# Kernel optimization log

Measured on AMD Instinct MI355X. Metric: run time of the kernel, lower is better.

## Reference

```python
import jax, jax.numpy as jnp
import numpy as np

EMB = 128
N_LIG = 32768
N_REC = 262144
NUM_GRAPHS = 1024
E_LIG = 327680
E_REC = 2097152
LIG_DIMS = [119, 9, 11, 12, 9, 5, 8, 2, 2]
NUM_LAYERS = 3
BN_EPS = 1e-5


def setup_inputs() -> dict:
    key = jax.random.key(0)
    ks = iter(jax.random.split(key, 64))

    lig_x = jnp.stack(
        [jax.random.randint(next(ks), (N_LIG,), 0, d) for d in LIG_DIMS], axis=1
    )  # [N_lig, 9] categorical atom features
    atom_offsets = jnp.asarray(np.cumsum([0] + LIG_DIMS[:-1]), dtype=jnp.int32)
    atom_emb = jax.random.normal(next(ks), (sum(LIG_DIMS), EMB), jnp.float32) * 0.1

    rec_x_int = jax.random.randint(next(ks), (N_REC,), 0, 20)
    rec_x_float = jax.random.normal(next(ks), (N_REC, 199), jnp.float32)
    rec_emb1 = jax.random.normal(next(ks), (20, EMB), jnp.float32) * 0.1
    rec_w = jax.random.normal(next(ks), (199, EMB), jnp.float32) * 0.05
    rec_b = jnp.zeros((EMB,), jnp.float32)

    lig_edge_index = jax.random.randint(next(ks), (2, E_LIG), 0, N_LIG)
    rec_edge_index = jax.random.randint(next(ks), (2, E_REC), 0, N_REC)
    lig_batch = jnp.repeat(jnp.arange(NUM_GRAPHS), N_LIG // NUM_GRAPHS)
    rec_batch = jnp.repeat(jnp.arange(NUM_GRAPHS), N_REC // NUM_GRAPHS)

    def layer_params():
        W = jax.random.normal(next(ks), (NUM_LAYERS, EMB, EMB), jnp.float32) * (1.0 / np.sqrt(EMB))
        b = jnp.zeros((NUM_LAYERS, EMB), jnp.float32)
        gamma = jnp.ones((NUM_LAYERS, EMB), jnp.float32)
        beta = jnp.zeros((NUM_LAYERS, EMB), jnp.float32)
        return W, b, gamma, beta

    lig_W, lig_b, lig_gamma, lig_beta = layer_params()
    rec_W, rec_bc, rec_gamma, rec_beta = layer_params()

    out_w1 = jax.random.normal(next(ks), (2 * EMB, EMB), jnp.float32) * (1.0 / np.sqrt(2 * EMB))
    out_b1 = jnp.zeros((EMB,), jnp.float32)
    out_w2 = jax.random.normal(next(ks), (EMB, 1), jnp.float32) * (1.0 / np.sqrt(EMB))
    out_b2 = jnp.zeros((1,), jnp.float32)

    return dict(
        lig_x=lig_x, rec_x_int=rec_x_int, rec_x_float=rec_x_float,
        lig_edge_index=lig_edge_index, rec_edge_index=rec_edge_index,
        lig_batch=lig_batch, rec_batch=rec_batch, atom_offsets=atom_offsets,
        atom_emb=atom_emb, rec_emb1=rec_emb1, rec_w=rec_w, rec_b=rec_b,
        lig_W=lig_W, lig_b=lig_b, lig_gamma=lig_gamma, lig_beta=lig_beta,
        rec_W=rec_W, rec_bc=rec_bc, rec_gamma=rec_gamma, rec_beta=rec_beta,
        out_w1=out_w1, out_b1=out_b1, out_w2=out_w2, out_b2=out_b2,
    )


def gcn_layer(x, edge_index, W, b, gamma, beta):
    """GCNConv (sym-norm, self loops) -> BatchNorm (batch stats) -> ReLU."""
    n = x.shape[0]
    h = x @ W  # [N, EMB]
    loops = jnp.arange(n)
    src = jnp.concatenate([edge_index[0], loops])
    dst = jnp.concatenate([edge_index[1], loops])
    deg = jax.ops.segment_sum(jnp.ones_like(dst, dtype=h.dtype), dst, num_segments=n)
    dinv = jax.lax.rsqrt(jnp.maximum(deg, 1.0))  # deg >= 1 with self loops
    msg = h[src] * (dinv[src] * dinv[dst])[:, None]  # gather + normalize
    out = jax.ops.segment_sum(msg, dst, num_segments=n) + b
    mu = out.mean(axis=0)
    var = out.var(axis=0)
    out = (out - mu) * jax.lax.rsqrt(var + BN_EPS) * gamma + beta
    return jax.nn.relu(out)


def scatter_mean(x, seg, num_segments):
    s = jax.ops.segment_sum(x, seg, num_segments=num_segments)
    cnt = jax.ops.segment_sum(jnp.ones((x.shape[0],), x.dtype), seg, num_segments=num_segments)
    return s / jnp.maximum(cnt, 1.0)[:, None]


def reference(lig_x, rec_x_int, rec_x_float, lig_edge_index, rec_edge_index,
              lig_batch, rec_batch, atom_offsets, atom_emb, rec_emb1, rec_w, rec_b,
              lig_W, lig_b, lig_gamma, lig_beta, rec_W, rec_bc, rec_gamma, rec_beta,
              out_w1, out_b1, out_w2, out_b2):
    # Node encoders
    lig_h = atom_emb[lig_x + atom_offsets[None, :]].sum(axis=1)        # [N_lig, EMB]
    rec_h = rec_emb1[rec_x_int] + rec_x_float @ rec_w + rec_b          # [N_rec, EMB]

    for l in range(NUM_LAYERS):
        lig_h = gcn_layer(lig_h, lig_edge_index, lig_W[l], lig_b[l], lig_gamma[l], lig_beta[l])
        rec_h = gcn_layer(rec_h, rec_edge_index, rec_W[l], rec_bc[l], rec_gamma[l], rec_beta[l])

    lig_feat = scatter_mean(lig_h, lig_batch, NUM_GRAPHS)
    rec_feat = scatter_mean(rec_h, rec_batch, NUM_GRAPHS)
    z = jnp.concatenate([lig_feat, rec_feat], axis=1)                  # [B, 2*EMB]
    z = jax.nn.relu(z @ out_w1 + out_b1)
    return (z @ out_w2 + out_b2).squeeze(-1)                            # [B]
```

## Files before the change

kernel.cpp:

```cpp
#include <hip/hip_runtime.h>
#include <hip/hip_bf16.h>
#include <cstdint>
#include <cstddef>

#define EMB 128
#define NLIG 32768
#define NREC 262144
#define NGRAPH 1024
#define ELIG 327680
#define EREC 2097152
#define BN_EPS 1e-5f

typedef unsigned short ushort_t;
typedef short bf16x8 __attribute__((ext_vector_type(8)));
typedef float f32x4 __attribute__((ext_vector_type(4)));

__device__ __forceinline__ float bf2f(ushort_t u) {
  union { unsigned int i; float f; } v;
  v.i = ((unsigned int)u) << 16;
  return v.f;
}
__device__ __forceinline__ ushort_t f2bf(float f) {
  __hip_bfloat16 h = __float2bfloat16(f);
  union { __hip_bfloat16 h; ushort_t u; } v;
  v.h = h;
  return v.u;
}


__global__ __launch_bounds__(256)
void gk_count(const int* __restrict__ dst, int* __restrict__ cnt, int E) {
  int e = blockIdx.x * 256 + threadIdx.x;
  if (e < E) atomicAdd(&cnt[dst[e]], 1);
}

__global__ __launch_bounds__(256)
void gk_scan1(const int* __restrict__ cnt, int* __restrict__ off,
              int* __restrict__ bsum, int n) {
  __shared__ int sm[256];
  int t = threadIdx.x;
  int base = blockIdx.x * 1024 + t * 4;
  int v0 = (base + 0 < n) ? cnt[base + 0] : 0;
  int v1 = (base + 1 < n) ? cnt[base + 1] : 0;
  int v2 = (base + 2 < n) ? cnt[base + 2] : 0;
  int v3 = (base + 3 < n) ? cnt[base + 3] : 0;
  int loc = v0 + v1 + v2 + v3;
  sm[t] = loc;
  __syncthreads();
  for (int o = 1; o < 256; o <<= 1) {
    int x = (t >= o) ? sm[t - o] : 0;
    __syncthreads();
    sm[t] += x;
    __syncthreads();
  }
  int run = sm[t] - loc;
  if (base + 0 < n) off[base + 0] = run;
  run += v0;
  if (base + 1 < n) off[base + 1] = run;
  run += v1;
  if (base + 2 < n) off[base + 2] = run;
  run += v2;
  if (base + 3 < n) off[base + 3] = run;
  if (t == 255) bsum[blockIdx.x] = sm[255];
}

__global__ __launch_bounds__(256)
void gk_scan2(int* __restrict__ bsum, int nb) {
  __shared__ int sm[256];
  int t = threadIdx.x;
  int v = (t < nb) ? bsum[t] : 0;
  sm[t] = v;
  __syncthreads();
  for (int o = 1; o < 256; o <<= 1) {
    int x = (t >= o) ? sm[t - o] : 0;
    __syncthreads();
    sm[t] += x;
    __syncthreads();
  }
  if (t < nb) bsum[t] = sm[t] - v;
}

__global__ __launch_bounds__(256)
void gk_scan3(int* __restrict__ off, const int* __restrict__ bsum, int n, int E) {
  int i = blockIdx.x * 256 + threadIdx.x;
  if (i < n) off[i] += bsum[i >> 10];
  if (i == 0) off[n] = E;
}

__global__ __launch_bounds__(256)
void gk_copy(int* __restrict__ d, const int* __restrict__ s, int n) {
  int i = blockIdx.x * 256 + threadIdx.x;
  if (i < n) d[i] = s[i];
}

__global__ __launch_bounds__(256)
void gk_fill(const int* __restrict__ src, const int* __restrict__ dst,
             int* __restrict__ cur, int* __restrict__ csr, int E) {
  int e = blockIdx.x * 256 + threadIdx.x;
  if (e < E) {
    int d = dst[e];
    int pos = atomicAdd(&cur[d], 1);
    csr[pos] = src[e];
  }
}

__global__ __launch_bounds__(256)
void gk_dinv(const int* __restrict__ off, float* __restrict__ dinv, int n) {
  int i = blockIdx.x * 256 + threadIdx.x;
  if (i < n) dinv[i] = rsqrtf((float)(off[i + 1] - off[i] + 1));
}


__global__ __launch_bounds__(128)
void gk_ligenc(const int* __restrict__ lig_x, const int* __restrict__ offs,
               const float* __restrict__ emb, ushort_t* __restrict__ A) {
  __shared__ int idx[9];
  int i = blockIdx.x;
  int c = threadIdx.x;
  if (c < 9) idx[c] = lig_x[i * 9 + c] + offs[c];
  __syncthreads();
  float acc = 0.f;
#pragma unroll
  for (int f = 0; f < 9; ++f) acc += emb[(size_t)idx[f] * EMB + c];
  A[(size_t)i * EMB + c] = f2bf(acc);
}

__global__ __launch_bounds__(256)
void gk_recw2(const float* __restrict__ W, ushort_t* __restrict__ Wt) {
  int idx = blockIdx.x * 256 + threadIdx.x;
  if (idx < 128 * 224) {
    int c = idx / 224, k = idx - c * 224;
    Wt[idx] = (k < 199) ? f2bf(W[(size_t)k * 128 + c]) : (ushort_t)0;
  }
}

__global__ __launch_bounds__(256)
void gk_xcast(const float* __restrict__ X, ushort_t* __restrict__ Xb) {
  const int ITEMS = NREC * 25;
  int stride = gridDim.x * 256;
  for (int v = blockIdx.x * 256 + threadIdx.x; v < ITEMS; v += stride) {
    int row = v / 25, sub = v - row * 25;
    int k0 = sub * 8;
    const float* xr = X + (size_t)row * 199 + k0;
    ushort_t tmp[8];
#pragma unroll
    for (int j = 0; j < 8; ++j) {
      float f = (k0 + j < 199) ? xr[j] : 0.f;
      tmp[j] = f2bf(f);
    }
    *(uint4*)(Xb + (size_t)row * 200 + k0) = *(uint4*)tmp;
  }
}

__global__ __launch_bounds__(256)
void gk_recenc2(const ushort_t* __restrict__ Xb, const int* __restrict__ xi,
                const float* __restrict__ emb1, const ushort_t* __restrict__ Wt,
                const float* __restrict__ b, ushort_t* __restrict__ A) {
  int t = threadIdx.x;
  int row0 = blockIdx.x * 128;
  int w = t >> 6, lane = t & 63;
  int m = lane & 15, quad = lane >> 4;
  int rbase = w * 32;
  int rA = row0 + rbase + m;
  int rB = rA + 16;

  f32x4 acc[2][8];
#pragma unroll
  for (int rt = 0; rt < 2; ++rt)
#pragma unroll
    for (int ct = 0; ct < 8; ++ct) acc[rt][ct] = (f32x4){0.f, 0.f, 0.f, 0.f};

  const ushort_t* xpA = Xb + (size_t)rA * 200 + quad * 8;
  const ushort_t* xpB = Xb + (size_t)rB * 200 + quad * 8;
  const ushort_t* wp = Wt + (size_t)m * 224 + quad * 8;

  for (int ch = 0; ch < 7; ++ch) {
    bf16x8 a0 = *(const bf16x8*)(xpA + ch * 32);
    bf16x8 a1 = *(const bf16x8*)(xpB + ch * 32);
#pragma unroll
    for (int ct = 0; ct < 8; ++ct) {
      bf16x8 bb = *(const bf16x8*)(wp + (size_t)ct * 16 * 224 + ch * 32);
      acc[0][ct] = __builtin_amdgcn_mfma_f32_16x16x32_bf16(a0, bb, acc[0][ct], 0, 0, 0);
      acc[1][ct] = __builtin_amdgcn_mfma_f32_16x16x32_bf16(a1, bb, acc[1][ct], 0, 0, 0);
    }
  }

  float bcol[8];
#pragma unroll
  for (int ct = 0; ct < 8; ++ct) bcol[ct] = b[ct * 16 + m];
#pragma unroll
  for (int rt = 0; rt < 2; ++rt) {
    int rb = row0 + rbase + rt * 16 + quad * 4;
#pragma unroll
    for (int rr = 0; rr < 4; ++rr) {
      int row = rb + rr;
      const float* e = emb1 + (size_t)xi[row] * 128;
#pragma unroll
      for (int ct = 0; ct < 8; ++ct) {
        int c = ct * 16 + m;
        float v = acc[rt][ct][rr] + bcol[ct] + e[c];
        A[(size_t)row * 128 + c] = f2bf(v);
      }
    }
  }
}

__global__ __launch_bounds__(256)
void gk_prep(const float* __restrict__ W, const float* __restrict__ stats,
             const float* __restrict__ gamma, const float* __restrict__ beta,
             float inv_n, int donorm, ushort_t* __restrict__ Wt,
             float* __restrict__ bnscl, float* __restrict__ bnsh) {
  int idx = blockIdx.x * 256 + threadIdx.x;
  if (idx < 128) {
    if (donorm) {
      float mu = stats[idx] * inv_n;
      float var = stats[128 + idx] * inv_n - mu * mu;
      float s = gamma[idx] * rsqrtf(var + BN_EPS);
      bnscl[idx] = s;
      bnsh[idx] = beta[idx] - mu * s;
    } else {
      bnscl[idx] = 1.f;
      bnsh[idx] = 0.f;
    }
  }
  int c = idx >> 7, k = idx & 127;
  Wt[(size_t)c * 128 + k] = f2bf(W[(size_t)k * 128 + c]);
}

__global__ __launch_bounds__(256)
void gk_mm(const ushort_t* __restrict__ Xb, const ushort_t* __restrict__ Wt,
           const float* __restrict__ bnscl, const float* __restrict__ bnsh,
           int donorm, const float* __restrict__ dinv,
           ushort_t* __restrict__ gb) {
  __shared__ ushort_t Xs[128 * 128];
  __shared__ ushort_t Ws[128 * 128];
  int t = threadIdx.x;
  int row0 = blockIdx.x * 128;

  for (int i = t; i < 2048; i += 256) {
    int r = i >> 4, cc = i & 15;
    union { uint4 v; ushort_t s[8]; } u;
    u.v = *(const uint4*)(Xb + (size_t)(row0 + r) * 128 + cc * 8);
    if (donorm) {
#pragma unroll
      for (int j = 0; j < 8; ++j) {
        int k = cc * 8 + j;
        float f = fmaf(bf2f(u.s[j]), bnscl[k], bnsh[k]);
        f = f > 0.f ? f : 0.f;
        u.s[j] = f2bf(f);
      }
    }
    *(uint4*)&Xs[r * 128 + ((cc ^ (r & 15)) * 8)] = u.v;
  }
  for (int i = t; i < 2048; i += 256) {
    int c = i >> 4, cc = i & 15;
    uint4 u = *(const uint4*)(Wt + (size_t)c * 128 + cc * 8);
    *(uint4*)&Ws[c * 128 + ((cc ^ (c & 15)) * 8)] = u;
  }
  __syncthreads();

  int w = t >> 6, lane = t & 63;
  int m = lane & 15, quad = lane >> 4;
  int rbase = w * 32;

  f32x4 acc[2][8];
#pragma unroll
  for (int rt = 0; rt < 2; ++rt)
#pragma unroll
    for (int ct = 0; ct < 8; ++ct) acc[rt][ct] = (f32x4){0.f, 0.f, 0.f, 0.f};

#pragma unroll
  for (int kc8 = 0; kc8 < 16; kc8 += 4) {
    int ck = (kc8 + quad) ^ m;
    bf16x8 a0 = *(const bf16x8*)&Xs[(rbase + m) * 128 + ck * 8];
    bf16x8 a1 = *(const bf16x8*)&Xs[(rbase + 16 + m) * 128 + ck * 8];
#pragma unroll
    for (int ct = 0; ct < 8; ++ct) {
      bf16x8 b = *(const bf16x8*)&Ws[(ct * 16 + m) * 128 + ck * 8];
      acc[0][ct] = __builtin_amdgcn_mfma_f32_16x16x32_bf16(a0, b, acc[0][ct], 0, 0, 0);
      acc[1][ct] = __builtin_amdgcn_mfma_f32_16x16x32_bf16(a1, b, acc[1][ct], 0, 0, 0);
    }
  }

#pragma unroll
  for (int rt = 0; rt < 2; ++rt) {
    int rb = row0 + rbase + rt * 16 + quad * 4;
    float d0 = dinv[rb + 0], d1 = dinv[rb + 1];
    float d2 = dinv[rb + 2], d3 = dinv[rb + 3];
#pragma unroll
    for (int ct = 0; ct < 8; ++ct) {
      int c = ct * 16 + m;
      gb[(size_t)(rb + 0) * 128 + c] = f2bf(acc[rt][ct][0] * d0);
      gb[(size_t)(rb + 1) * 128 + c] = f2bf(acc[rt][ct][1] * d1);
      gb[(size_t)(rb + 2) * 128 + c] = f2bf(acc[rt][ct][2] * d2);
      gb[(size_t)(rb + 3) * 128 + c] = f2bf(acc[rt][ct][3] * d3);
    }
  }
}


struct Quad {
  int i0, i1, i2, i3;
  float m0, m1, m2, m3;
};

__device__ __forceinline__ Quad load_quad(const int* __restrict__ csr,
                                          int e, int e1, int safe) {
  Quad q;
  int c0 = (e + 0 < e1) ? e + 0 : safe;
  int c1 = (e + 1 < e1) ? e + 1 : safe;
  int c2 = (e + 2 < e1) ? e + 2 : safe;
  int c3 = (e + 3 < e1) ? e + 3 : safe;
  q.i0 = csr[c0];
  q.i1 = csr[c1];
  q.i2 = csr[c2];
  q.i3 = csr[c3];
  q.m0 = (e + 0 < e1) ? 1.f : 0.f;
  q.m1 = (e + 1 < e1) ? 1.f : 0.f;
  q.m2 = (e + 2 < e1) ? 1.f : 0.f;
  q.m3 = (e + 3 < e1) ? 1.f : 0.f;
  return q;
}

__device__ __forceinline__ void gather4(const ushort_t* __restrict__ g, int c0,
                                        const Quad& q, unsigned int* v) {
  v[0] = *(const unsigned int*)(g + (size_t)q.i0 * 128 + c0);
  v[1] = *(const unsigned int*)(g + (size_t)q.i1 * 128 + c0);
  v[2] = *(const unsigned int*)(g + (size_t)q.i2 * 128 + c0);
  v[3] = *(const unsigned int*)(g + (size_t)q.i3 * 128 + c0);
}

__device__ __forceinline__ void consume4(float2& acc, const Quad& q,
                                         const unsigned int* v) {
  float lo0 = bf2f((ushort_t)(v[0] & 0xffffu)), hi0 = bf2f((ushort_t)(v[0] >> 16));
  float lo1 = bf2f((ushort_t)(v[1] & 0xffffu)), hi1 = bf2f((ushort_t)(v[1] >> 16));
  float lo2 = bf2f((ushort_t)(v[2] & 0xffffu)), hi2 = bf2f((ushort_t)(v[2] >> 16));
  float lo3 = bf2f((ushort_t)(v[3] & 0xffffu)), hi3 = bf2f((ushort_t)(v[3] >> 16));
  acc.x = fmaf(lo0, q.m0, acc.x); acc.y = fmaf(hi0, q.m0, acc.y);
  acc.x = fmaf(lo1, q.m1, acc.x); acc.y = fmaf(hi1, q.m1, acc.y);
  acc.x = fmaf(lo2, q.m2, acc.x); acc.y = fmaf(hi2, q.m2, acc.y);
  acc.x = fmaf(lo3, q.m3, acc.x); acc.y = fmaf(hi3, q.m3, acc.y);
}

__global__ __launch_bounds__(256)
void gk_agg(const ushort_t* __restrict__ g, const int* __restrict__ off,
            const int* __restrict__ csr, const float* __restrict__ dinv,
            ushort_t* __restrict__ outb, float* __restrict__ stats) {
  __shared__ float ls[128];
  __shared__ float lss[128];
  int t = threadIdx.x;
  int slot = t >> 6;
  int lane = t & 63;
  int c0 = lane * 2;
  int i0 = blockIdx.x * 32;

  if (t < 128) { ls[t] = 0.f; lss[t] = 0.f; }
  __syncthreads();

  float sx = 0.f, sy = 0.f, ssx = 0.f, ssy = 0.f;

  for (int p = 0; p < 4; ++p) {
    int rA = i0 + slot * 2 + p * 8;
    int rB = rA + 1;
    int eA = off[rA], eA1 = off[rA + 1];
    int eB1 = off[rB + 1];
    int eB = eA1;
    float dA = dinv[rA], dB = dinv[rB];
    unsigned int uA = *(const unsigned int*)(g + (size_t)rA * 128 + c0);
    unsigned int uB = *(const unsigned int*)(g + (size_t)rB * 128 + c0);
    float2 accA = make_float2(bf2f((ushort_t)(uA & 0xffffu)),
                              bf2f((ushort_t)(uA >> 16)));
    float2 accB = make_float2(bf2f((ushort_t)(uB & 0xffffu)),
                              bf2f((ushort_t)(uB >> 16)));
    int safeA = (eA1 > eA) ? eA1 - 1 : 0;
    int safeB = (eB1 > eB) ? eB1 - 1 : 0;

    Quad qA = load_quad(csr, eA, eA1, safeA);
    Quad qB = load_quad(csr, eB, eB1, safeB);
    unsigned int vA[4], vB[4];
    gather4(g, c0, qA, vA);
    gather4(g, c0, qB, vB);
    int e_A = eA + 4, e_B = eB + 4;

    while (e_A < eA1 || e_B < eB1) {
      bool an = e_A < eA1;
      bool bn = e_B < eB1;
      Quad qA2, qB2;
      unsigned int wA[4], wB[4];
      if (an) {
        qA2 = load_quad(csr, e_A, eA1, safeA);
        gather4(g, c0, qA2, wA);
      }
      if (bn) {
        qB2 = load_quad(csr, e_B, eB1, safeB);
        gather4(g, c0, qB2, wB);
      }
      consume4(accA, qA, vA);
      consume4(accB, qB, vB);
      if (an) {
        qA = qA2; vA[0] = wA[0]; vA[1] = wA[1]; vA[2] = wA[2]; vA[3] = wA[3];
        e_A += 4;
      } else {
        qA.m0 = qA.m1 = qA.m2 = qA.m3 = 0.f;
      }
      if (bn) {
        qB = qB2; vB[0] = wB[0]; vB[1] = wB[1]; vB[2] = wB[2]; vB[3] = wB[3];
        e_B += 4;
      } else {
        qB.m0 = qB.m1 = qB.m2 = qB.m3 = 0.f;
      }
    }
    consume4(accA, qA, vA);
    consume4(accB, qB, vB);

    accA.x *= dA; accA.y *= dA;
    accB.x *= dB; accB.y *= dB;
    unsigned int oA = (unsigned int)f2bf(accA.x) | ((unsigned int)f2bf(accA.y) << 16);
    unsigned int oB = (unsigned int)f2bf(accB.x) | ((unsigned int)f2bf(accB.y) << 16);
    *(unsigned int*)(outb + (size_t)rA * 128 + c0) = oA;
    *(unsigned int*)(outb + (size_t)rB * 128 + c0) = oB;
    sx += accA.x + accB.x;
    sy += accA.y + accB.y;
    ssx = fmaf(accA.x, accA.x, ssx); ssx = fmaf(accB.x, accB.x, ssx);
    ssy = fmaf(accA.y, accA.y, ssy); ssy = fmaf(accB.y, accB.y, ssy);
  }

  atomicAdd(&ls[c0 + 0], sx);
  atomicAdd(&ls[c0 + 1], sy);
  atomicAdd(&lss[c0 + 0], ssx);
  atomicAdd(&lss[c0 + 1], ssy);
  __syncthreads();
  if (t < 128) {
    atomicAdd(&stats[t], ls[t]);
    atomicAdd(&stats[t + 128], lss[t]);
  }
}

__global__ __launch_bounds__(128)
void gk_pool(const ushort_t* __restrict__ A, const float* __restrict__ stats,
             const float* __restrict__ gamma, const float* __restrict__ beta,
             float inv_n, float* __restrict__ z, int npg, int zoff) {
  int gidx = blockIdx.x;
  int c = threadIdx.x;
  float mu = stats[c] * inv_n;
  float var = stats[128 + c] * inv_n - mu * mu;
  float scl = gamma[c] * rsqrtf(var + BN_EPS);
  float be = beta[c];
  float sum = 0.f;
  int r0 = gidx * npg;
  for (int r = 0; r < npg; ++r) {
    float v = (bf2f(A[(size_t)(r0 + r) * 128 + c]) - mu) * scl + be;
    sum += v > 0.f ? v : 0.f;
  }
  z[(size_t)gidx * 256 + zoff + c] = sum * (1.0f / (float)npg);
}

__global__ __launch_bounds__(128)
void gk_mlp(const float* __restrict__ z, const float* __restrict__ w1,
            const float* __restrict__ b1, const float* __restrict__ w2,
            const float* __restrict__ b2, float* __restrict__ out) {
  __shared__ float zs[256];
  __shared__ float red[128];
  int gidx = blockIdx.x, t = threadIdx.x;
  zs[t] = z[(size_t)gidx * 256 + t];
  zs[t + 128] = z[(size_t)gidx * 256 + 128 + t];
  __syncthreads();
  float acc = b1[t];
  for (int k = 0; k < 256; ++k) acc += zs[k] * w1[(size_t)k * 128 + t];
  acc = (acc > 0.f ? acc : 0.f) * w2[t];
  red[t] = acc;
  __syncthreads();
  for (int o = 64; o > 0; o >>= 1) {
    if (t < o) red[t] += red[t + o];
    __syncthreads();
  }
  if (t == 0) out[gidx] = red[0] + b2[0];
}


extern "C" void kernel_launch(void* const* d_in, const int* in_sizes, int n_in,
                              void* d_out, int out_size, void* d_ws, size_t ws_size,
                              hipStream_t stream) {
  (void)in_sizes; (void)n_in; (void)out_size; (void)ws_size;
  const int*   lig_x       = (const int*)  d_in[0];
  const int*   rec_x_int   = (const int*)  d_in[1];
  const float* rec_x_float = (const float*)d_in[2];
  const int*   lig_ei      = (const int*)  d_in[3];
  const int*   rec_ei      = (const int*)  d_in[4];
  const int*   atom_off    = (const int*)  d_in[7];
  const float* atom_emb    = (const float*)d_in[8];
  const float* rec_emb1    = (const float*)d_in[9];
  const float* rec_w       = (const float*)d_in[10];
  const float* rec_b       = (const float*)d_in[11];
  const float* lig_W       = (const float*)d_in[12];
  const float* lig_gamma   = (const float*)d_in[14];
  const float* lig_beta    = (const float*)d_in[15];
  const float* rec_W       = (const float*)d_in[16];
  const float* rec_gamma   = (const float*)d_in[18];
  const float* rec_beta    = (const float*)d_in[19];
  const float* out_w1      = (const float*)d_in[20];
  const float* out_b1      = (const float*)d_in[21];
  const float* out_w2      = (const float*)d_in[22];
  const float* out_b2      = (const float*)d_in[23];
  float* out = (float*)d_out;

  char* p = (char*)d_ws;
  auto alloc = [&](size_t bytes) -> void* {
    void* r = p;
    p += (bytes + 255) & ~(size_t)255;
    return r;
  };
  ushort_t* Ab     = (ushort_t*)alloc((size_t)NREC * EMB * 2);
  ushort_t* Gb     = (ushort_t*)alloc((size_t)NREC * EMB * 2);
  ushort_t* Wtb    = (ushort_t*)alloc((size_t)EMB * EMB * 2);
  ushort_t* WtK    = (ushort_t*)alloc((size_t)EMB * 224 * 2);
  ushort_t* Xb2    = (ushort_t*)alloc(((size_t)NREC * 200 + 64) * 2);
  float* bnscl     = (float*)alloc(128 * 4);
  float* bnsh      = (float*)alloc(128 * 4);
  float* dinv_lig  = (float*)alloc((size_t)NLIG * 4);
  float* dinv_rec  = (float*)alloc((size_t)NREC * 4);
  int*   cnt_lig   = (int*)  alloc((size_t)NLIG * 4);
  int*   cnt_rec   = (int*)  alloc((size_t)NREC * 4);
  int*   off_lig   = (int*)  alloc((size_t)(NLIG + 1) * 4);
  int*   off_rec   = (int*)  alloc((size_t)(NREC + 1) * 4);
  int*   csr_lig   = (int*)  alloc((size_t)ELIG * 4);
  int*   csr_rec   = (int*)  alloc((size_t)EREC * 4);
  int*   bsum_lig  = (int*)  alloc(256 * 4);
  int*   bsum_rec  = (int*)  alloc(256 * 4);
  float* stats     = (float*)alloc(256 * 4);
  float* z         = (float*)alloc((size_t)NGRAPH * 256 * 4);

  hipMemsetAsync(cnt_lig, 0, (size_t)NLIG * 4, stream);
  hipMemsetAsync(cnt_rec, 0, (size_t)NREC * 4, stream);
  gk_count<<<ELIG / 256, 256, 0, stream>>>(lig_ei + ELIG, cnt_lig, ELIG);
  gk_count<<<EREC / 256, 256, 0, stream>>>(rec_ei + EREC, cnt_rec, EREC);
  gk_scan1<<<NLIG / 1024, 256, 0, stream>>>(cnt_lig, off_lig, bsum_lig, NLIG);
  gk_scan2<<<1, 256, 0, stream>>>(bsum_lig, NLIG / 1024);
  gk_scan3<<<NLIG / 256, 256, 0, stream>>>(off_lig, bsum_lig, NLIG, ELIG);
  gk_scan1<<<NREC / 1024, 256, 0, stream>>>(cnt_rec, off_rec, bsum_rec, NREC);
  gk_scan2<<<1, 256, 0, stream>>>(bsum_rec, NREC / 1024);
  gk_scan3<<<NREC / 256, 256, 0, stream>>>(off_rec, bsum_rec, NREC, EREC);
  gk_copy<<<NLIG / 256, 256, 0, stream>>>(cnt_lig, off_lig, NLIG);
  gk_copy<<<NREC / 256, 256, 0, stream>>>(cnt_rec, off_rec, NREC);
  gk_fill<<<ELIG / 256, 256, 0, stream>>>(lig_ei, lig_ei + ELIG, cnt_lig, csr_lig, ELIG);
  gk_fill<<<EREC / 256, 256, 0, stream>>>(rec_ei, rec_ei + EREC, cnt_rec, csr_rec, EREC);
  gk_dinv<<<NLIG / 256, 256, 0, stream>>>(off_lig, dinv_lig, NLIG);
  gk_dinv<<<NREC / 256, 256, 0, stream>>>(off_rec, dinv_rec, NREC);

  auto run_entity = [&](const float* Wall, const float* gamma, const float* beta,
                        const int* offv, const int* csrv, const float* dinv,
                        int n, int npg, int zoff) {
    float inv_n = 1.0f / (float)n;
    for (int l = 0; l < 3; ++l) {
      const float* W = Wall + (size_t)l * EMB * EMB;
      const float* gm = (l > 0) ? gamma + (size_t)(l - 1) * EMB : gamma;
      const float* bt = (l > 0) ? beta + (size_t)(l - 1) * EMB : beta;
      gk_prep<<<64, 256, 0, stream>>>(W, stats, gm, bt, inv_n, l > 0 ? 1 : 0,
                                      Wtb, bnscl, bnsh);
      hipMemsetAsync(stats, 0, 256 * 4, stream);
      gk_mm<<<n / 128, 256, 0, stream>>>(Ab, Wtb, bnscl, bnsh, l > 0 ? 1 : 0,
                                         dinv, Gb);
      gk_agg<<<n / 32, 256, 0, stream>>>(Gb, offv, csrv, dinv, Ab, stats);
    }
    gk_pool<<<NGRAPH, 128, 0, stream>>>(Ab, stats, gamma + 2 * EMB, beta + 2 * EMB,
                                        inv_n, z, npg, zoff);
  };

  gk_ligenc<<<NLIG, 128, 0, stream>>>(lig_x, atom_off, atom_emb, Ab);
  run_entity(lig_W, lig_gamma, lig_beta, off_lig, csr_lig, dinv_lig,
             NLIG, NLIG / NGRAPH, 0);

  gk_recw2<<<112, 256, 0, stream>>>(rec_w, WtK);
  gk_xcast<<<2048, 256, 0, stream>>>(rec_x_float, Xb2);
  gk_recenc2<<<NREC / 128, 256, 0, stream>>>(Xb2, rec_x_int, rec_emb1,
                                             WtK, rec_b, Ab);
  run_entity(rec_W, rec_gamma, rec_beta, off_rec, csr_rec, dinv_rec,
             NREC, NREC / NGRAPH, EMB);

  gk_mlp<<<NGRAPH, 128, 0, stream>>>(z, out_w1, out_b1, out_w2, out_b2, out);
}
```

Before: 1.900 ms.

## Widen aggregation gathers to 8 bytes and use a uniform loop bound

The GCN aggregation kernel now has each lane gather four bf16 channels (uint2) instead of two, so half a wavefront covers a 128-wide row and a wavefront handles four rows, two per half. Each block covers 16 rows instead of 32, and the grid is doubled. The per-row while loop with divergent branches becomes a uniform loop bounded by the maximum degree among the four rows, with masking for inactive edges. This trades wasted masked gathers on uneven-degree rows for fewer, wider memory requests and less branching. It also reads a few extra offset entries, so the offset buffers are padded.

```diff
diff --git a/kernel.cpp b/kernel.cpp
--- a/kernel.cpp
+++ b/kernel.cpp
@@ -300,46 +300,42 @@
 
 
 struct Quad {
-  int i0, i1, i2, i3;
-  float m0, m1, m2, m3;
+  int i[4];
+  float m[4];
 };
 
 __device__ __forceinline__ Quad load_quad(const int* __restrict__ csr,
                                           int e, int e1, int safe) {
   Quad q;
-  int c0 = (e + 0 < e1) ? e + 0 : safe;
-  int c1 = (e + 1 < e1) ? e + 1 : safe;
-  int c2 = (e + 2 < e1) ? e + 2 : safe;
-  int c3 = (e + 3 < e1) ? e + 3 : safe;
-  q.i0 = csr[c0];
-  q.i1 = csr[c1];
-  q.i2 = csr[c2];
-  q.i3 = csr[c3];
-  q.m0 = (e + 0 < e1) ? 1.f : 0.f;
-  q.m1 = (e + 1 < e1) ? 1.f : 0.f;
-  q.m2 = (e + 2 < e1) ? 1.f : 0.f;
-  q.m3 = (e + 3 < e1) ? 1.f : 0.f;
+#pragma unroll
+  for (int j = 0; j < 4; ++j) {
+    int c = (e + j < e1) ? e + j : safe;
+    q.i[j] = csr[c];
+    q.m[j] = (e + j < e1) ? 1.f : 0.f;
+  }
   return q;
 }
 
-__device__ __forceinline__ void gather4(const ushort_t* __restrict__ g, int c0,
-                                        const Quad& q, unsigned int* v) {
-  v[0] = *(const unsigned int*)(g + (size_t)q.i0 * 128 + c0);
-  v[1] = *(const unsigned int*)(g + (size_t)q.i1 * 128 + c0);
-  v[2] = *(const unsigned int*)(g + (size_t)q.i2 * 128 + c0);
-  v[3] = *(const unsigned int*)(g + (size_t)q.i3 * 128 + c0);
-}
-
-__device__ __forceinline__ void consume4(float2& acc, const Quad& q,
-                                         const unsigned int* v) {
-  float lo0 = bf2f((ushort_t)(v[0] & 0xffffu)), hi0 = bf2f((ushort_t)(v[0] >> 16));
-  float lo1 = bf2f((ushort_t)(v[1] & 0xffffu)), hi1 = bf2f((ushort_t)(v[1] >> 16));
-  float lo2 = bf2f((ushort_t)(v[2] & 0xffffu)), hi2 = bf2f((ushort_t)(v[2] >> 16));
-  float lo3 = bf2f((ushort_t)(v[3] & 0xffffu)), hi3 = bf2f((ushort_t)(v[3] >> 16));
-  acc.x = fmaf(lo0, q.m0, acc.x); acc.y = fmaf(hi0, q.m0, acc.y);
-  acc.x = fmaf(lo1, q.m1, acc.x); acc.y = fmaf(hi1, q.m1, acc.y);
-  acc.x = fmaf(lo2, q.m2, acc.x); acc.y = fmaf(hi2, q.m2, acc.y);
-  acc.x = fmaf(lo3, q.m3, acc.x); acc.y = fmaf(hi3, q.m3, acc.y);
+__device__ __forceinline__ void gather4w(const ushort_t* __restrict__ g, int c0,
+                                         const Quad& q, uint2* v) {
+#pragma unroll
+  for (int j = 0; j < 4; ++j)
+    v[j] = *(const uint2*)(g + (size_t)q.i[j] * 128 + c0);
+}
+
+__device__ __forceinline__ void consume4w(float* acc, const Quad& q,
+                                          const uint2* v) {
+#pragma unroll
+  for (int j = 0; j < 4; ++j) {
+    float x0 = bf2f((ushort_t)(v[j].x & 0xffffu));
+    float x1 = bf2f((ushort_t)(v[j].x >> 16));
+    float x2 = bf2f((ushort_t)(v[j].y & 0xffffu));
+    float x3 = bf2f((ushort_t)(v[j].y >> 16));
+    acc[0] = fmaf(x0, q.m[j], acc[0]);
+    acc[1] = fmaf(x1, q.m[j], acc[1]);
+    acc[2] = fmaf(x2, q.m[j], acc[2]);
+    acc[3] = fmaf(x3, q.m[j], acc[3]);
+  }
 }
 
 __global__ __launch_bounds__(256)
@@ -349,86 +345,85 @@
   __shared__ float ls[128];
   __shared__ float lss[128];
   int t = threadIdx.x;
-  int slot = t >> 6;
+  int w = t >> 6;
   int lane = t & 63;
-  int c0 = lane * 2;
-  int i0 = blockIdx.x * 32;
+  int h = lane >> 5;
+  int sl = lane & 31;
+  int c0 = sl * 4;
+  int r0 = blockIdx.x * 16 + w * 4;
 
   if (t < 128) { ls[t] = 0.f; lss[t] = 0.f; }
   __syncthreads();
 
-  float sx = 0.f, sy = 0.f, ssx = 0.f, ssy = 0.f;
-
-  for (int p = 0; p < 4; ++p) {
-    int rA = i0 + slot * 2 + p * 8;
-    int rB = rA + 1;
-    int eA = off[rA], eA1 = off[rA + 1];
-    int eB1 = off[rB + 1];
-    int eB = eA1;
-    float dA = dinv[rA], dB = dinv[rB];
-    unsigned int uA = *(const unsigned int*)(g + (size_t)rA * 128 + c0);
-    unsigned int uB = *(const unsigned int*)(g + (size_t)rB * 128 + c0);
-    float2 accA = make_float2(bf2f((ushort_t)(uA & 0xffffu)),
-                              bf2f((ushort_t)(uA >> 16)));
-    float2 accB = make_float2(bf2f((ushort_t)(uB & 0xffffu)),
-                              bf2f((ushort_t)(uB >> 16)));
-    int safeA = (eA1 > eA) ? eA1 - 1 : 0;
-    int safeB = (eB1 > eB) ? eB1 - 1 : 0;
-
-    Quad qA = load_quad(csr, eA, eA1, safeA);
-    Quad qB = load_quad(csr, eB, eB1, safeB);
-    unsigned int vA[4], vB[4];
-    gather4(g, c0, qA, vA);
-    gather4(g, c0, qB, vB);
-    int e_A = eA + 4, e_B = eB + 4;
-
-    while (e_A < eA1 || e_B < eB1) {
-      bool an = e_A < eA1;
-      bool bn = e_B < eB1;
-      Quad qA2, qB2;
-      unsigned int wA[4], wB[4];
-      if (an) {
-        qA2 = load_quad(csr, e_A, eA1, safeA);
-        gather4(g, c0, qA2, wA);
-      }
-      if (bn) {
-        qB2 = load_quad(csr, e_B, eB1, safeB);
-        gather4(g, c0, qB2, wB);
-      }
-      consume4(accA, qA, vA);
-      consume4(accB, qB, vB);
-      if (an) {
-        qA = qA2; vA[0] = wA[0]; vA[1] = wA[1]; vA[2] = wA[2]; vA[3] = wA[3];
-        e_A += 4;
-      } else {
-        qA.m0 = qA.m1 = qA.m2 = qA.m3 = 0.f;
-      }
-      if (bn) {
-        qB = qB2; vB[0] = wB[0]; vB[1] = wB[1]; vB[2] = wB[2]; vB[3] = wB[3];
-        e_B += 4;
-      } else {
-        qB.m0 = qB.m1 = qB.m2 = qB.m3 = 0.f;
-      }
-    }
-    consume4(accA, qA, vA);
-    consume4(accB, qB, vB);
-
-    accA.x *= dA; accA.y *= dA;
-    accB.x *= dB; accB.y *= dB;
-    unsigned int oA = (unsigned int)f2bf(accA.x) | ((unsigned int)f2bf(accA.y) << 16);
-    unsigned int oB = (unsigned int)f2bf(accB.x) | ((unsigned int)f2bf(accB.y) << 16);
-    *(unsigned int*)(outb + (size_t)rA * 128 + c0) = oA;
-    *(unsigned int*)(outb + (size_t)rB * 128 + c0) = oB;
-    sx += accA.x + accB.x;
-    sy += accA.y + accB.y;
-    ssx = fmaf(accA.x, accA.x, ssx); ssx = fmaf(accB.x, accB.x, ssx);
-    ssy = fmaf(accA.y, accA.y, ssy); ssy = fmaf(accB.y, accB.y, ssy);
-  }
-
-  atomicAdd(&ls[c0 + 0], sx);
-  atomicAdd(&ls[c0 + 1], sy);
-  atomicAdd(&lss[c0 + 0], ssx);
-  atomicAdd(&lss[c0 + 1], ssy);
+  int o0 = off[r0 + 0], o1 = off[r0 + 1], o2 = off[r0 + 2];
+  int o3 = off[r0 + 3], o4 = off[r0 + 4];
+  int maxd = max(max(o1 - o0, o2 - o1), max(o3 - o2, o4 - o3));
+
+  int u = r0 + h * 2;
+  int v = u + 1;
+  int eU = h ? o2 : o0, eU1 = h ? o3 : o1;
+  int eV = h ? o3 : o1, eV1 = h ? o4 : o2;
+  float dU = dinv[u], dV = dinv[v];
+
+  uint2 sU = *(const uint2*)(g + (size_t)u * 128 + c0);
+  uint2 sV = *(const uint2*)(g + (size_t)v * 128 + c0);
+  float accU[4], accV[4];
+  accU[0] = bf2f((ushort_t)(sU.x & 0xffffu));
+  accU[1] = bf2f((ushort_t)(sU.x >> 16));
+  accU[2] = bf2f((ushort_t)(sU.y & 0xffffu));
+  accU[3] = bf2f((ushort_t)(sU.y >> 16));
+  accV[0] = bf2f((ushort_t)(sV.x & 0xffffu));
+  accV[1] = bf2f((ushort_t)(sV.x >> 16));
+  accV[2] = bf2f((ushort_t)(sV.y & 0xffffu));
+  accV[3] = bf2f((ushort_t)(sV.y >> 16));
+
+  int safeU = (eU1 > eU) ? eU1 - 1 : 0;
+  int safeV = (eV1 > eV) ? eV1 - 1 : 0;
+
+  Quad qU = load_quad(csr, eU, eU1, safeU);
+  Quad qV = load_quad(csr, eV, eV1, safeV);
+  uint2 vU[4], vV[4];
+  gather4w(g, c0, qU, vU);
+  gather4w(g, c0, qV, vV);
+  int eUc = eU + 4, eVc = eV + 4;
+
+  int rem = (maxd > 4) ? ((maxd - 1) >> 2) : 0;
+  for (int it = 0; it < rem; ++it) {
+    Quad nU = load_quad(csr, eUc, eU1, safeU);
+    Quad nV = load_quad(csr, eVc, eV1, safeV);
+    uint2 wU[4], wV[4];
+    gather4w(g, c0, nU, wU);
+    gather4w(g, c0, nV, wV);
+    consume4w(accU, qU, vU);
+    consume4w(accV, qV, vV);
+    qU = nU; qV = nV;
+#pragma unroll
+    for (int j = 0; j < 4; ++j) { vU[j] = wU[j]; vV[j] = wV[j]; }
+    eUc += 4; eVc += 4;
+  }
+  consume4w(accU, qU, vU);
+  consume4w(accV, qV, vV);
+
+  float sx[4], ssx[4];
+#pragma unroll
+  for (int k = 0; k < 4; ++k) {
+    accU[k] *= dU; accV[k] *= dV;
+    sx[k] = accU[k] + accV[k];
+    ssx[k] = fmaf(accU[k], accU[k], accV[k] * accV[k]);
+  }
+  uint2 oU, oV;
+  oU.x = (unsigned int)f2bf(accU[0]) | ((unsigned int)f2bf(accU[1]) << 16);
+  oU.y = (unsigned int)f2bf(accU[2]) | ((unsigned int)f2bf(accU[3]) << 16);
+  oV.x = (unsigned int)f2bf(accV[0]) | ((unsigned int)f2bf(accV[1]) << 16);
+  oV.y = (unsigned int)f2bf(accV[2]) | ((unsigned int)f2bf(accV[3]) << 16);
+  *(uint2*)(outb + (size_t)u * 128 + c0) = oU;
+  *(uint2*)(outb + (size_t)v * 128 + c0) = oV;
+
+#pragma unroll
+  for (int k = 0; k < 4; ++k) {
+    atomicAdd(&ls[c0 + k], sx[k]);
+    atomicAdd(&lss[c0 + k], ssx[k]);
+  }
   __syncthreads();
   if (t < 128) {
     atomicAdd(&stats[t], ls[t]);
@@ -521,8 +516,8 @@
   float* dinv_rec  = (float*)alloc((size_t)NREC * 4);
   int*   cnt_lig   = (int*)  alloc((size_t)NLIG * 4);
   int*   cnt_rec   = (int*)  alloc((size_t)NREC * 4);
-  int*   off_lig   = (int*)  alloc((size_t)(NLIG + 1) * 4);
-  int*   off_rec   = (int*)  alloc((size_t)(NREC + 1) * 4);
+  int*   off_lig   = (int*)  alloc((size_t)(NLIG + 8) * 4);
+  int*   off_rec   = (int*)  alloc((size_t)(NREC + 8) * 4);
   int*   csr_lig   = (int*)  alloc((size_t)ELIG * 4);
   int*   csr_rec   = (int*)  alloc((size_t)EREC * 4);
   int*   bsum_lig  = (int*)  alloc(256 * 4);
@@ -532,6 +527,8 @@
 
   hipMemsetAsync(cnt_lig, 0, (size_t)NLIG * 4, stream);
   hipMemsetAsync(cnt_rec, 0, (size_t)NREC * 4, stream);
+  hipMemsetAsync(off_lig + NLIG + 1, 0, 7 * 4, stream);
+  hipMemsetAsync(off_rec + NREC + 1, 0, 7 * 4, stream);
   gk_count<<<ELIG / 256, 256, 0, stream>>>(lig_ei + ELIG, cnt_lig, ELIG);
   gk_count<<<EREC / 256, 256, 0, stream>>>(rec_ei + EREC, cnt_rec, EREC);
   gk_scan1<<<NLIG / 1024, 256, 0, stream>>>(cnt_lig, off_lig, bsum_lig, NLIG);
@@ -560,7 +557,7 @@
       hipMemsetAsync(stats, 0, 256 * 4, stream);
       gk_mm<<<n / 128, 256, 0, stream>>>(Ab, Wtb, bnscl, bnsh, l > 0 ? 1 : 0,
                                          dinv, Gb);
-      gk_agg<<<n / 32, 256, 0, stream>>>(Gb, offv, csrv, dinv, Ab, stats);
+      gk_agg<<<n / 16, 256, 0, stream>>>(Gb, offv, csrv, dinv, Ab, stats);
     }
     gk_pool<<<NGRAPH, 128, 0, stream>>>(Ab, stats, gamma + 2 * EMB, beta + 2 * EMB,
                                         inv_n, z, npg, zoff);
```

Result: slower. 2.663 ms (+40.2%).

## Preload CSR neighbor indices per wave and broadcast via shuffles in aggregation

Applied to the files above, without the earlier changes.

The aggregation kernel now loads the block's row offsets and up to 64 neighbor indices per row cooperatively across the wave, one per lane, and broadcasts them with __shfl. The old path had every lane redundantly load each index. Gathers are issued in batches of 8 with double buffering instead of 4. Rows with more than 64 neighbors fall back to a serial loop. This removes redundant scalar index loads and deepens memory-level parallelism, at the cost of more registers and shuffle overhead, plus a slow tail path for high-degree nodes.

```diff
diff --git a/kernel.cpp b/kernel.cpp
--- a/kernel.cpp
+++ b/kernel.cpp
@@ -299,47 +299,23 @@
 }
 
 
-struct Quad {
-  int i0, i1, i2, i3;
-  float m0, m1, m2, m3;
-};
-
-__device__ __forceinline__ Quad load_quad(const int* __restrict__ csr,
-                                          int e, int e1, int safe) {
-  Quad q;
-  int c0 = (e + 0 < e1) ? e + 0 : safe;
-  int c1 = (e + 1 < e1) ? e + 1 : safe;
-  int c2 = (e + 2 < e1) ? e + 2 : safe;
-  int c3 = (e + 3 < e1) ? e + 3 : safe;
-  q.i0 = csr[c0];
-  q.i1 = csr[c1];
-  q.i2 = csr[c2];
-  q.i3 = csr[c3];
-  q.m0 = (e + 0 < e1) ? 1.f : 0.f;
-  q.m1 = (e + 1 < e1) ? 1.f : 0.f;
-  q.m2 = (e + 2 < e1) ? 1.f : 0.f;
-  q.m3 = (e + 3 < e1) ? 1.f : 0.f;
-  return q;
-}
-
-__device__ __forceinline__ void gather4(const ushort_t* __restrict__ g, int c0,
-                                        const Quad& q, unsigned int* v) {
-  v[0] = *(const unsigned int*)(g + (size_t)q.i0 * 128 + c0);
-  v[1] = *(const unsigned int*)(g + (size_t)q.i1 * 128 + c0);
-  v[2] = *(const unsigned int*)(g + (size_t)q.i2 * 128 + c0);
-  v[3] = *(const unsigned int*)(g + (size_t)q.i3 * 128 + c0);
-}
-
-__device__ __forceinline__ void consume4(float2& acc, const Quad& q,
-                                         const unsigned int* v) {
-  float lo0 = bf2f((ushort_t)(v[0] & 0xffffu)), hi0 = bf2f((ushort_t)(v[0] >> 16));
-  float lo1 = bf2f((ushort_t)(v[1] & 0xffffu)), hi1 = bf2f((ushort_t)(v[1] >> 16));
-  float lo2 = bf2f((ushort_t)(v[2] & 0xffffu)), hi2 = bf2f((ushort_t)(v[2] >> 16));
-  float lo3 = bf2f((ushort_t)(v[3] & 0xffffu)), hi3 = bf2f((ushort_t)(v[3] >> 16));
-  acc.x = fmaf(lo0, q.m0, acc.x); acc.y = fmaf(hi0, q.m0, acc.y);
-  acc.x = fmaf(lo1, q.m1, acc.x); acc.y = fmaf(hi1, q.m1, acc.y);
-  acc.x = fmaf(lo2, q.m2, acc.x); acc.y = fmaf(hi2, q.m2, acc.y);
-  acc.x = fmaf(lo3, q.m3, acc.x); acc.y = fmaf(hi3, q.m3, acc.y);
+__device__ __forceinline__ void gather8(const ushort_t* __restrict__ g, int c0,
+                                        int idxv, int q, unsigned int* v) {
+#pragma unroll
+  for (int k = 0; k < 8; ++k) {
+    int idx = __shfl(idxv, q * 8 + k);
+    v[k] = *(const unsigned int*)(g + (size_t)idx * 128 + c0);
+  }
+}
+
+__device__ __forceinline__ void consume8(float2& acc, const unsigned int* v,
+                                         int q, int deg) {
+#pragma unroll
+  for (int k = 0; k < 8; ++k) {
+    float m = (q * 8 + k < deg) ? 1.f : 0.f;
+    acc.x = fmaf(bf2f((ushort_t)(v[k] & 0xffffu)), m, acc.x);
+    acc.y = fmaf(bf2f((ushort_t)(v[k] >> 16)), m, acc.y);
+  }
 }
 
 __global__ __launch_bounds__(256)
@@ -357,61 +333,76 @@
   if (t < 128) { ls[t] = 0.f; lss[t] = 0.f; }
   __syncthreads();
 
+  int offv = off[i0 + min(lane, 32)];
+
+  int idxA[4], idxB[4], dAs[4], dBs[4];
+#pragma unroll
+  for (int p = 0; p < 4; ++p) {
+    int base = slot * 2 + p * 8;
+    int eA  = __shfl(offv, base + 0);
+    int eB  = __shfl(offv, base + 1);
+    int eB1 = __shfl(offv, base + 2);
+    dAs[p] = eB - eA;
+    dBs[p] = eB1 - eB;
+    int adrA = (dAs[p] > 0) ? min(eA + lane, eB - 1) : 0;
+    int adrB = (dBs[p] > 0) ? min(eB + lane, eB1 - 1) : 0;
+    idxA[p] = csr[adrA];
+    idxB[p] = csr[adrB];
+  }
+
   float sx = 0.f, sy = 0.f, ssx = 0.f, ssy = 0.f;
 
+#pragma unroll
   for (int p = 0; p < 4; ++p) {
     int rA = i0 + slot * 2 + p * 8;
     int rB = rA + 1;
-    int eA = off[rA], eA1 = off[rA + 1];
-    int eB1 = off[rB + 1];
-    int eB = eA1;
+    int degA = dAs[p], degB = dBs[p];
     float dA = dinv[rA], dB = dinv[rB];
-    unsigned int uA = *(const unsigned int*)(g + (size_t)rA * 128 + c0);
-    unsigned int uB = *(const unsigned int*)(g + (size_t)rB * 128 + c0);
-    float2 accA = make_float2(bf2f((ushort_t)(uA & 0xffffu)),
-                              bf2f((ushort_t)(uA >> 16)));
-    float2 accB = make_float2(bf2f((ushort_t)(uB & 0xffffu)),
-                              bf2f((ushort_t)(uB >> 16)));
-    int safeA = (eA1 > eA) ? eA1 - 1 : 0;
-    int safeB = (eB1 > eB) ? eB1 - 1 : 0;
-
-    Quad qA = load_quad(csr, eA, eA1, safeA);
-    Quad qB = load_quad(csr, eB, eB1, safeB);
-    unsigned int vA[4], vB[4];
-    gather4(g, c0, qA, vA);
-    gather4(g, c0, qB, vB);
-    int e_A = eA + 4, e_B = eB + 4;
-
-    while (e_A < eA1 || e_B < eB1) {
-      bool an = e_A < eA1;
-      bool bn = e_B < eB1;
-      Quad qA2, qB2;
-      unsigned int wA[4], wB[4];
-      if (an) {
-        qA2 = load_quad(csr, e_A, eA1, safeA);
-        gather4(g, c0, qA2, wA);
+
+    unsigned int sU = *(const unsigned int*)(g + (size_t)rA * 128 + c0);
+    unsigned int sV = *(const unsigned int*)(g + (size_t)rB * 128 + c0);
+    float2 accA = make_float2(bf2f((ushort_t)(sU & 0xffffu)),
+                              bf2f((ushort_t)(sU >> 16)));
+    float2 accB = make_float2(bf2f((ushort_t)(sV & 0xffffu)),
+                              bf2f((ushort_t)(sV >> 16)));
+
+    int dAf = min(degA, 64), dBf = min(degB, 64);
+    int nc = (max(dAf, dBf) + 7) >> 3;
+    if (nc > 0) {
+      unsigned int vA[8], vB[8];
+      gather8(g, c0, idxA[p], 0, vA);
+      gather8(g, c0, idxB[p], 0, vB);
+      for (int q = 1; q < nc; ++q) {
+        unsigned int wA[8], wB[8];
+        gather8(g, c0, idxA[p], q, wA);
+        gather8(g, c0, idxB[p], q, wB);
+        consume8(accA, vA, q - 1, dAf);
+        consume8(accB, vB, q - 1, dBf);
+#pragma unroll
+        for (int k = 0; k < 8; ++k) { vA[k] = wA[k]; vB[k] = wB[k]; }
       }
-      if (bn) {
-        qB2 = load_quad(csr, e_B, eB1, safeB);
-        gather4(g, c0, qB2, wB);
+      consume8(accA, vA, nc - 1, dAf);
+      consume8(accB, vB, nc - 1, dBf);
+    }
+
+    if (degA > 64) {
+      int eA = __shfl(offv, slot * 2 + p * 8);
+      for (int e = eA + 64; e < eA + degA; ++e) {
+        int idx = csr[e];
+        unsigned int v = *(const unsigned int*)(g + (size_t)idx * 128 + c0);
+        accA.x += bf2f((ushort_t)(v & 0xffffu));
+        accA.y += bf2f((ushort_t)(v >> 16));
       }
-      consume4(accA, qA, vA);
-      consume4(accB, qB, vB);
-      if (an) {
-        qA = qA2; vA[0] = wA[0]; vA[1] = wA[1]; vA[2] = wA[2]; vA[3] = wA[3];
-        e_A += 4;
-      } else {
-        qA.m0 = qA.m1 = qA.m2 = qA.m3 = 0.f;
+    }
+    if (degB > 64) {
+      int eB = __shfl(offv, slot * 2 + p * 8 + 1);
+      for (int e = eB + 64; e < eB + degB; ++e) {
+        int idx = csr[e];
+        unsigned int v = *(const unsigned int*)(g + (size_t)idx * 128 + c0);
+        accB.x += bf2f((ushort_t)(v & 0xffffu));
+        accB.y += bf2f((ushort_t)(v >> 16));
       }
-      if (bn) {
-        qB = qB2; vB[0] = wB[0]; vB[1] = wB[1]; vB[2] = wB[2]; vB[3] = wB[3];
-        e_B += 4;
-      } else {
-        qB.m0 = qB.m1 = qB.m2 = qB.m3 = 0.f;
-      }
-    }
-    consume4(accA, qA, vA);
-    consume4(accB, qB, vB);
+    }
 
     accA.x *= dA; accA.y *= dA;
     accB.x *= dB; accB.y *= dB;
@@ -521,8 +512,8 @@
   float* dinv_rec  = (float*)alloc((size_t)NREC * 4);
   int*   cnt_lig   = (int*)  alloc((size_t)NLIG * 4);
   int*   cnt_rec   = (int*)  alloc((size_t)NREC * 4);
-  int*   off_lig   = (int*)  alloc((size_t)(NLIG + 1) * 4);
-  int*   off_rec   = (int*)  alloc((size_t)(NREC + 1) * 4);
+  int*   off_lig   = (int*)  alloc((size_t)(NLIG + 8) * 4);
+  int*   off_rec   = (int*)  alloc((size_t)(NREC + 8) * 4);
   int*   csr_lig   = (int*)  alloc((size_t)ELIG * 4);
   int*   csr_rec   = (int*)  alloc((size_t)EREC * 4);
   int*   bsum_lig  = (int*)  alloc(256 * 4);
```

After: 1.879 ms. No clear change (-1.1%).
